# Optimization experiments

Measured on AMD Instinct MI355X. Metric: run time of the kernel, lower is better.

The kernel has to match this reference:

```python
import jax, jax.numpy as jnp
import numpy as np

N, E, D, R = 50000, 600000, 128, 8


def rgcn_conv(x, src, dst, etype, W, root, bias):
    """PyG-style RGCNConv with mean aggregation per relation.
    x: [N, Din]; W: [R, Din, Dout]; root: [Din, Dout]; bias: [Dout]."""
    n = x.shape[0]
    r = W.shape[0]
    # Transform once per relation at node level (cheaper than per-edge matmul).
    xw = jnp.einsum('nd,rdo->rno', x, W)  # [R, N, Dout]
    # Per-(relation, target) edge counts for mean normalization.
    seg = etype * n + dst                  # combined segment id in [0, R*N)
    counts = jax.ops.segment_sum(jnp.ones(src.shape, dtype=x.dtype), seg,
                                 num_segments=r * n)
    norm = 1.0 / jnp.maximum(counts[seg], 1.0)   # [E]
    msg = xw[etype, src] * norm[:, None]          # gather per edge, [E, Dout]
    agg = jax.ops.segment_sum(msg, dst, num_segments=n)  # scatter-add, [N, Dout]
    return agg + x @ root + bias


def setup_inputs() -> dict:
    key = jax.random.key(0)
    ks = jax.random.split(key, 16)
    s = 1.0 / np.sqrt(D)
    inp = {
        'x': jax.random.normal(ks[0], (N, D), dtype=jnp.float32),
        'edge_index': jax.random.randint(ks[1], (2, E), 0, N, dtype=jnp.int32),
        'edge_type': jax.random.randint(ks[2], (E,), 0, R, dtype=jnp.int32),
        'W1': jax.random.normal(ks[3], (R, D, D), dtype=jnp.float32) * s,
        'root1': jax.random.normal(ks[4], (D, D), dtype=jnp.float32) * s,
        'b1': jnp.zeros((D,), dtype=jnp.float32),
        'W2': jax.random.normal(ks[5], (R, D, D), dtype=jnp.float32) * s,
        'root2': jax.random.normal(ks[6], (D, D), dtype=jnp.float32) * s,
        'b2': jnp.zeros((D,), dtype=jnp.float32),
        'W3': jax.random.normal(ks[7], (R, D, D), dtype=jnp.float32) * s,
        'root3': jax.random.normal(ks[8], (D, D), dtype=jnp.float32) * s,
        'b3': jnp.zeros((D,), dtype=jnp.float32),
        'res_w': jax.random.normal(ks[9], (D, D), dtype=jnp.float32) * s,
        'res_b': jnp.zeros((D,), dtype=jnp.float32),
    }
    return inp


def reference(x, edge_index, edge_type, W1, root1, b1, W2, root2, b2,
              W3, root3, b3, res_w, res_b):
    src, dst = edge_index[0], edge_index[1]
    res = x @ res_w + res_b
    h = jax.nn.relu(rgcn_conv(x, src, dst, edge_type, W1, root1, b1))
    h = res + jax.nn.relu(h)
    h = jax.nn.relu(rgcn_conv(h, src, dst, edge_type, W2, root2, b2))
    h = res + jax.nn.relu(h)
    h = jax.nn.relu(rgcn_conv(h, src, dst, edge_type, W3, root3, b3))
    h = res + jax.nn.relu(h)
    # Dropout(0.05) is identity in eval mode.
    return h
```

## Files before the change

### kernel.cpp

```cpp
#include <hip/hip_runtime.h>
#include <hip/hip_bf16.h>

#define NN 50000
#define EE 600000
#define RR 8
#define NSEG (NN*RR)
#define NB_SCAN ((NSEG + 1023)/1024)

typedef unsigned int u32;
typedef __attribute__((ext_vector_type(8))) short bf16x8;
typedef __attribute__((ext_vector_type(4))) float f32x4;
typedef __attribute__((ext_vector_type(4))) u32 u32x4;

__device__ inline unsigned short f2bf(float f){
  u32 u = __float_as_uint(f);
  u32 r = (u + 0x7fffu + ((u >> 16) & 1u)) >> 16;
  return (unsigned short)r;
}
__device__ inline float bf2f(unsigned short b){ return __uint_as_float((u32)b << 16); }

#define GLD16(g, l)  __builtin_amdgcn_global_load_lds( \
    (const __attribute__((address_space(1))) void*)(g), \
    (__attribute__((address_space(3))) void*)(l), 16, 0, 0)

__global__ void cvt_k(const float* __restrict__ in, unsigned short* __restrict__ out, int n4){
  int i = blockIdx.x * 256 + threadIdx.x;
  if (i >= n4) return;
  float4 v = ((const float4*)in)[i];
  ushort4 o;
  o.x = f2bf(v.x); o.y = f2bf(v.y); o.z = f2bf(v.z); o.w = f2bf(v.w);
  ((ushort4*)out)[i] = o;
}

__global__ void pack_k(const float* __restrict__ Wrel, const float* __restrict__ root,
                       short* __restrict__ Bp, int nk32, int krel){
  int tid = blockIdx.x * 256 + threadIdx.x;
  if (tid >= nk32 * 512) return;
  int lane = tid & 63;
  int nf   = (tid >> 6) & 7;
  int k32  = tid >> 9;
  int col  = nf * 16 + (lane & 15);
  short vals[8];
#pragma unroll
  for (int i = 0; i < 8; ++i){
    int kk = k32 * 32 + ((lane >> 4) << 3) + i;
    float f = (kk < krel) ? Wrel[(size_t)kk * 128 + col]
                          : root[(size_t)(kk - krel) * 128 + col];
    vals[i] = (short)f2bf(f);
  }
  *(bf16x8*)(Bp + (size_t)tid * 8) = *(const bf16x8*)vals;
}

__global__ void count_k(const int* __restrict__ dst, const int* __restrict__ et,
                        u32* __restrict__ cnt){
  int e = blockIdx.x * 256 + threadIdx.x;
  if (e >= EE) return;
  atomicAdd(&cnt[(size_t)et[e] * NN + dst[e]], 1u);
}

__global__ void scan1_k(const u32* __restrict__ cnt, u32* __restrict__ offs, u32* __restrict__ bsum){
  __shared__ u32 s[512];
  int t = threadIdx.x;
  int base = blockIdx.x * 1024 + t * 4;
  u32 loc[4]; u32 sum = 0;
#pragma unroll
  for (int i = 0; i < 4; ++i){ loc[i] = (base + i < NSEG) ? cnt[base + i] : 0u; sum += loc[i]; }
  int pb = 0;
  s[t] = sum; __syncthreads();
  for (int off = 1; off < 256; off <<= 1){
    u32 v = s[pb * 256 + t];
    if (t >= off) v += s[pb * 256 + t - off];
    s[(pb ^ 1) * 256 + t] = v; pb ^= 1; __syncthreads();
  }
  u32 incl = s[pb * 256 + t];
  u32 excl = incl - sum;
  if (t == 255) bsum[blockIdx.x] = incl;
  u32 run = excl;
#pragma unroll
  for (int i = 0; i < 4; ++i){ if (base + i < NSEG) offs[base + i] = run; run += loc[i]; }
}

__global__ void scan2_k(u32* __restrict__ bsum){
  __shared__ u32 s[1024];
  int t = threadIdx.x;
  u32 v = (t < NB_SCAN) ? bsum[t] : 0u;
  int pb = 0;
  s[t] = v; __syncthreads();
  for (int off = 1; off < 512; off <<= 1){
    u32 x = s[pb * 512 + t];
    if (t >= off) x += s[pb * 512 + t - off];
    s[(pb ^ 1) * 512 + t] = x; pb ^= 1; __syncthreads();
  }
  u32 incl = s[pb * 512 + t];
  if (t < NB_SCAN) bsum[t] = incl - v;
}

__global__ void scan3_k(u32* __restrict__ offs, const u32* __restrict__ bsum){
  int t = threadIdx.x;
  int base = blockIdx.x * 1024 + t * 4;
  u32 add = bsum[blockIdx.x];
#pragma unroll
  for (int i = 0; i < 4; ++i){ if (base + i < NSEG) offs[base + i] += add; }
  if (blockIdx.x == 0 && t == 0) offs[NSEG] = EE;
}

__global__ void fill_k(const int* __restrict__ src, const int* __restrict__ dst,
                       const int* __restrict__ et, const u32* __restrict__ offs,
                       u32* __restrict__ cnt, int* __restrict__ elist){
  int e = blockIdx.x * 256 + threadIdx.x;
  if (e >= EE) return;
  int s = et[e] * NN + dst[e];
  u32 p = atomicSub(&cnt[s], 1u);
  elist[offs[s] + p - 1] = src[e];
}

__launch_bounds__(256, 4)
__global__ void resg_k(const unsigned short* __restrict__ xb, const short* __restrict__ Bp,
                       const float* __restrict__ rb, unsigned short* __restrict__ resb){
  const int tid = threadIdx.x;
  const int w = tid >> 6, l = tid & 63;
  const int sub = l >> 4, llr = l & 15;
  const int rowbase = blockIdx.x * 64 + w * 16;
  int vr = rowbase + llr; if (vr > NN - 1) vr = NN - 1;
  f32x4 acc[8] = {};
#pragma unroll
  for (int t = 0; t < 4; ++t){
    bf16x8 af = *(const bf16x8*)(xb + (size_t)vr * 128 + (t * 4 + sub) * 8);
    const short* bb = Bp + (size_t)(t * 8) * 512 + l * 8;
#pragma unroll
    for (int nf = 0; nf < 8; ++nf){
      bf16x8 bq = *(const bf16x8*)(bb + nf * 512);
      acc[nf] = __builtin_amdgcn_mfma_f32_16x16x32_bf16(af, bq, acc[nf], 0, 0, 0);
    }
  }
  const int lr = l >> 4, lc = l & 15;
#pragma unroll
  for (int nf = 0; nf < 8; ++nf){
    int col = nf * 16 + lc;
    float bv = rb[col];
#pragma unroll
    for (int r = 0; r < 4; ++r){
      int row = rowbase + lr * 4 + r;
      if (row < NN) resb[(size_t)row * 128 + col] = f2bf(acc[nf][r] + bv);
    }
  }
}

#define ACC1(P0, P1) do{ \
  _Pragma("unroll") \
  for (int i_ = 0; i_ < 4; ++i_){ \
    s[2*i_]     += __uint_as_float((P0)[i_] << 16); \
    s[2*i_+1]   += __uint_as_float((P0)[i_] & 0xffff0000u); \
    s[8+2*i_]   += __uint_as_float((P1)[i_] << 16); \
    s[8+2*i_+1] += __uint_as_float((P1)[i_] & 0xffff0000u); \
  } }while(0)

template<int OUTMODE>
__launch_bounds__(512, 4)
__global__ void fused_k(const u32* __restrict__ offs, const int* __restrict__ elist,
                        const unsigned short* __restrict__ h,
                        const short* __restrict__ Bp,
                        const float* __restrict__ bias,
                        const unsigned short* __restrict__ resb,
                        float* __restrict__ outf, unsigned short* __restrict__ outb){
  __shared__ short A[32 * 1152];
  char* Ab = (char*)A;
  const int tid = threadIdx.x;
  const int mbase = blockIdx.x * 32;

  {
    const int g = tid >> 3, ll8 = tid & 7;
    const unsigned short* hb = h + (size_t)ll8 * 16;
#pragma unroll 1
    for (int j = 0; j < 5; ++j){
      int task = j * 64 + g;
      if (task < 256){
        int r = task >> 5, row = task & 31;
        int v = mbase + row; if (v > NN - 1) v = NN - 1;
        size_t seg = (size_t)r * NN + v;
        u32 beg = offs[seg], end = offs[seg + 1];
        float s[16];
#pragma unroll
        for (int i = 0; i < 16; ++i) s[i] = 0.f;
        u32 e = beg;
        for (; e + 4 <= end; e += 4){
          int s0 = elist[e], s1 = elist[e+1], s2 = elist[e+2], s3 = elist[e+3];
          const unsigned short* r0 = hb + (size_t)s0 * 128;
          const unsigned short* r1 = hb + (size_t)s1 * 128;
          const unsigned short* r2 = hb + (size_t)s2 * 128;
          const unsigned short* r3 = hb + (size_t)s3 * 128;
          u32x4 p00 = *(const u32x4*)r0, p01 = *(const u32x4*)(r0 + 8);
          u32x4 p10 = *(const u32x4*)r1, p11 = *(const u32x4*)(r1 + 8);
          u32x4 p20 = *(const u32x4*)r2, p21 = *(const u32x4*)(r2 + 8);
          u32x4 p30 = *(const u32x4*)r3, p31 = *(const u32x4*)(r3 + 8);
          ACC1(p00, p01); ACC1(p10, p11); ACC1(p20, p21); ACC1(p30, p31);
        }
        if (e + 2 <= end){
          int s0 = elist[e], s1 = elist[e+1];
          const unsigned short* r0 = hb + (size_t)s0 * 128;
          const unsigned short* r1 = hb + (size_t)s1 * 128;
          u32x4 p00 = *(const u32x4*)r0, p01 = *(const u32x4*)(r0 + 8);
          u32x4 p10 = *(const u32x4*)r1, p11 = *(const u32x4*)(r1 + 8);
          ACC1(p00, p01); ACC1(p10, p11);
          e += 2;
        }
        if (e < end){
          int s0 = elist[e];
          const unsigned short* r0 = hb + (size_t)s0 * 128;
          u32x4 p00 = *(const u32x4*)r0, p01 = *(const u32x4*)(r0 + 8);
          ACC1(p00, p01);
        }
        u32 deg = end - beg;
        if (deg){
          float inv = 1.f / (float)deg;
#pragma unroll
          for (int i = 0; i < 16; ++i) s[i] *= inv;
        }
        u32x4 o0, o1;
#pragma unroll
        for (int i = 0; i < 4; ++i){
          o0[i] = (u32)f2bf(s[2*i])   | ((u32)f2bf(s[2*i+1])   << 16);
          o1[i] = (u32)f2bf(s[8+2*i]) | ((u32)f2bf(s[8+2*i+1]) << 16);
        }
        int k = row & 7;
        int sl = r * 16 + ll8 * 2;
        *(u32x4*)(Ab + row * 2304 + ((sl    ) ^ k) * 16) = o0;
        *(u32x4*)(Ab + row * 2304 + ((sl + 1) ^ k) * 16) = o1;
      } else if (task < 288){
        int row = task - 256;
        int v = mbase + row; if (v > NN - 1) v = NN - 1;
        const unsigned short* rp = h + (size_t)v * 128 + ll8 * 16;
        u32x4 o0 = *(const u32x4*)rp, o1 = *(const u32x4*)(rp + 8);
        int k = row & 7;
        int sl = 128 + ll8 * 2;
        *(u32x4*)(Ab + row * 2304 + ((sl    ) ^ k) * 16) = o0;
        *(u32x4*)(Ab + row * 2304 + ((sl + 1) ^ k) * 16) = o1;
      }
    }
  }
  __syncthreads();

  const int w = tid >> 6, l = tid & 63;
  const int sub = l >> 4, llr = l & 15;
  f32x4 acc[2] = {};
  const int k0 = llr & 7, k1 = (16 + llr) & 7;
#pragma unroll 6
  for (int kt = 0; kt < 18; ++kt){
#pragma unroll
    for (int t = 0; t < 2; ++t){
      int ks = kt * 8 + t * 4 + sub;
      bf16x8 af0 = *(const bf16x8*)(Ab + llr * 2304        + (ks ^ k0) * 16);
      bf16x8 af1 = *(const bf16x8*)(Ab + (16 + llr) * 2304 + (ks ^ k1) * 16);
      bf16x8 bq = *(const bf16x8*)(Bp + ((size_t)((kt * 2 + t) * 8 + w)) * 512 + l * 8);
      acc[0] = __builtin_amdgcn_mfma_f32_16x16x32_bf16(af0, bq, acc[0], 0, 0, 0);
      acc[1] = __builtin_amdgcn_mfma_f32_16x16x32_bf16(af1, bq, acc[1], 0, 0, 0);
    }
  }

  const int lr = l >> 4, lc = l & 15;
  int col = w * 16 + lc;
  float bv = bias[col];
#pragma unroll
  for (int mf = 0; mf < 2; ++mf){
#pragma unroll
    for (int r = 0; r < 4; ++r){
      int row = mbase + mf * 16 + lr * 4 + r;
      if (row < NN){
        float v = acc[mf][r] + bv;
        v = bf2f(resb[(size_t)row * 128 + col]) + fmaxf(v, 0.f);
        if (OUTMODE == 1) outb[(size_t)row * 128 + col] = f2bf(v);
        else              outf[(size_t)row * 128 + col] = v;
      }
    }
  }
}

extern "C" void kernel_launch(void* const* d_in, const int* in_sizes, int n_in,
                              void* d_out, int out_size, void* d_ws, size_t ws_size,
                              hipStream_t stream){
  const float* x  = (const float*)d_in[0];
  const int*   ei = (const int*)d_in[1];
  const int*   et = (const int*)d_in[2];
  const float* W1 = (const float*)d_in[3];
  const float* r1 = (const float*)d_in[4];
  const float* b1 = (const float*)d_in[5];
  const float* W2 = (const float*)d_in[6];
  const float* r2 = (const float*)d_in[7];
  const float* b2 = (const float*)d_in[8];
  const float* W3 = (const float*)d_in[9];
  const float* r3 = (const float*)d_in[10];
  const float* b3 = (const float*)d_in[11];
  const float* rw = (const float*)d_in[12];
  const float* rb = (const float*)d_in[13];
  const int* srcv = ei;
  const int* dstv = ei + EE;

  char* p = (char*)d_ws;
  auto take = [&](size_t b)->char*{ char* q = p; p += (b + 255) & ~(size_t)255; return q; };
  unsigned short* xb   = (unsigned short*)take((size_t)NN * 128 * 2);
  unsigned short* h1   = (unsigned short*)take((size_t)NN * 128 * 2);
  unsigned short* h2   = (unsigned short*)take((size_t)NN * 128 * 2);
  unsigned short* resb = (unsigned short*)take((size_t)NN * 128 * 2);
  short* Bp1 = (short*)take(36 * 4096 * 2);
  short* Bp2 = (short*)take(36 * 4096 * 2);
  short* Bp3 = (short*)take(36 * 4096 * 2);
  short* BpR = (short*)take(4 * 4096 * 2);
  u32* cnt   = (u32*)take((size_t)NSEG * 4);
  u32* offs  = (u32*)take((size_t)(NSEG + 1) * 4);
  int* elist = (int*)take((size_t)EE * 4);
  u32* bsum  = (u32*)take((size_t)NB_SCAN * 4);

  hipMemsetAsync(cnt, 0, (size_t)NSEG * 4, stream);

  cvt_k<<<(NN * 128 / 4 + 255) / 256, 256, 0, stream>>>(x, xb, NN * 128 / 4);
  pack_k<<<(36 * 512 + 255) / 256, 256, 0, stream>>>(W1, r1, Bp1, 36, 1024);
  pack_k<<<(36 * 512 + 255) / 256, 256, 0, stream>>>(W2, r2, Bp2, 36, 1024);
  pack_k<<<(36 * 512 + 255) / 256, 256, 0, stream>>>(W3, r3, Bp3, 36, 1024);
  pack_k<<<(4 * 512 + 255) / 256, 256, 0, stream>>>(nullptr, rw, BpR, 4, 0);

  count_k<<<(EE + 255) / 256, 256, 0, stream>>>(dstv, et, cnt);
  scan1_k<<<NB_SCAN, 256, 0, stream>>>(cnt, offs, bsum);
  scan2_k<<<1, 512, 0, stream>>>(bsum);
  scan3_k<<<NB_SCAN, 256, 0, stream>>>(offs, bsum);
  fill_k<<<(EE + 255) / 256, 256, 0, stream>>>(srcv, dstv, et, offs, cnt, elist);

  const int GB = (NN + 31) / 32;

  resg_k<<<(NN + 63) / 64, 256, 0, stream>>>(xb, BpR, rb, resb);

  fused_k<1><<<GB, 512, 0, stream>>>(offs, elist, xb, Bp1, b1, resb, nullptr, h1);
  fused_k<1><<<GB, 512, 0, stream>>>(offs, elist, h1, Bp2, b2, resb, nullptr, h2);
  fused_k<2><<<GB, 512, 0, stream>>>(offs, elist, h2, Bp3, b3, resb, (float*)d_out, nullptr);
}
```

Before: 316.6 us.

## Widen fused RGCN blocks to 1024 threads with one-shot gather and padded LDS

The fused gather+GEMM kernel now uses 1024 threads per block. Each 8-lane group handles exactly two (relation,row) segments with a software-prefetched gather loop, replacing the 5-iteration task loop. The LDS tile switches from an XOR swizzle to a padded row stride. Each wave now computes one 16x16 MFMA tile instead of two, and the four weight-packing launches are merged into one kernel. The aim is more parallelism and latency hiding in the gather and fewer launches, at the cost of a shallower per-segment unroll and lower per-wave MFMA reuse of the B fragments.

```diff
diff --git a/kernel.cpp b/kernel.cpp
--- a/kernel.cpp
+++ b/kernel.cpp
@@ -6,6 +6,7 @@
 #define RR 8
 #define NSEG (NN*RR)
 #define NB_SCAN ((NSEG + 1023)/1024)
+#define RSTRIDE 2320
 
 typedef unsigned int u32;
 typedef __attribute__((ext_vector_type(8))) short bf16x8;
@@ -18,10 +19,6 @@
   return (unsigned short)r;
 }
 __device__ inline float bf2f(unsigned short b){ return __uint_as_float((u32)b << 16); }
-
-#define GLD16(g, l)  __builtin_amdgcn_global_load_lds( \
-    (const __attribute__((address_space(1))) void*)(g), \
-    (__attribute__((address_space(3))) void*)(l), 16, 0, 0)
 
 __global__ void cvt_k(const float* __restrict__ in, unsigned short* __restrict__ out, int n4){
   int i = blockIdx.x * 256 + threadIdx.x;
@@ -32,13 +29,22 @@
   ((ushort4*)out)[i] = o;
 }
 
-__global__ void pack_k(const float* __restrict__ Wrel, const float* __restrict__ root,
-                       short* __restrict__ Bp, int nk32, int krel){
+__global__ void packall_k(const float* __restrict__ W1, const float* __restrict__ r1,
+                          const float* __restrict__ W2, const float* __restrict__ r2,
+                          const float* __restrict__ W3, const float* __restrict__ r3,
+                          const float* __restrict__ rw,
+                          short* __restrict__ Bp1, short* __restrict__ Bp2,
+                          short* __restrict__ Bp3, short* __restrict__ BpR){
   int tid = blockIdx.x * 256 + threadIdx.x;
-  if (tid >= nk32 * 512) return;
+  if (tid >= 112 * 512) return;
+  int unit = tid >> 9;
+  const float* Wrel; const float* root; short* Bp; int k32; int krel;
+  if      (unit < 36){ Wrel = W1; root = r1; Bp = Bp1; k32 = unit;       krel = 1024; }
+  else if (unit < 72){ Wrel = W2; root = r2; Bp = Bp2; k32 = unit - 36;  krel = 1024; }
+  else if (unit <108){ Wrel = W3; root = r3; Bp = Bp3; k32 = unit - 72;  krel = 1024; }
+  else               { Wrel = rw; root = rw; Bp = BpR; k32 = unit - 108; krel = 0;    }
   int lane = tid & 63;
   int nf   = (tid >> 6) & 7;
-  int k32  = tid >> 9;
   int col  = nf * 16 + (lane & 15);
   short vals[8];
 #pragma unroll
@@ -48,7 +54,7 @@
                           : root[(size_t)(kk - krel) * 128 + col];
     vals[i] = (short)f2bf(f);
   }
-  *(bf16x8*)(Bp + (size_t)tid * 8) = *(const bf16x8*)vals;
+  *(bf16x8*)(Bp + (size_t)(k32 * 512 + (tid & 511)) * 8) = *(const bf16x8*)vals;
 }
 
 __global__ void count_k(const int* __restrict__ dst, const int* __restrict__ et,
@@ -156,121 +162,102 @@
   } }while(0)
 
 template<int OUTMODE>
-__launch_bounds__(512, 4)
+__launch_bounds__(1024, 8)
 __global__ void fused_k(const u32* __restrict__ offs, const int* __restrict__ elist,
                         const unsigned short* __restrict__ h,
                         const short* __restrict__ Bp,
                         const float* __restrict__ bias,
                         const unsigned short* __restrict__ resb,
                         float* __restrict__ outf, unsigned short* __restrict__ outb){
-  __shared__ short A[32 * 1152];
-  char* Ab = (char*)A;
+  __shared__ char Ab[32 * RSTRIDE];
   const int tid = threadIdx.x;
   const int mbase = blockIdx.x * 32;
 
   {
     const int g = tid >> 3, ll8 = tid & 7;
     const unsigned short* hb = h + (size_t)ll8 * 16;
-#pragma unroll 1
-    for (int j = 0; j < 5; ++j){
-      int task = j * 64 + g;
-      if (task < 256){
-        int r = task >> 5, row = task & 31;
-        int v = mbase + row; if (v > NN - 1) v = NN - 1;
-        size_t seg = (size_t)r * NN + v;
-        u32 beg = offs[seg], end = offs[seg + 1];
-        float s[16];
-#pragma unroll
-        for (int i = 0; i < 16; ++i) s[i] = 0.f;
-        u32 e = beg;
-        for (; e + 4 <= end; e += 4){
-          int s0 = elist[e], s1 = elist[e+1], s2 = elist[e+2], s3 = elist[e+3];
-          const unsigned short* r0 = hb + (size_t)s0 * 128;
-          const unsigned short* r1 = hb + (size_t)s1 * 128;
-          const unsigned short* r2 = hb + (size_t)s2 * 128;
-          const unsigned short* r3 = hb + (size_t)s3 * 128;
-          u32x4 p00 = *(const u32x4*)r0, p01 = *(const u32x4*)(r0 + 8);
-          u32x4 p10 = *(const u32x4*)r1, p11 = *(const u32x4*)(r1 + 8);
-          u32x4 p20 = *(const u32x4*)r2, p21 = *(const u32x4*)(r2 + 8);
-          u32x4 p30 = *(const u32x4*)r3, p31 = *(const u32x4*)(r3 + 8);
-          ACC1(p00, p01); ACC1(p10, p11); ACC1(p20, p21); ACC1(p30, p31);
-        }
-        if (e + 2 <= end){
-          int s0 = elist[e], s1 = elist[e+1];
-          const unsigned short* r0 = hb + (size_t)s0 * 128;
-          const unsigned short* r1 = hb + (size_t)s1 * 128;
-          u32x4 p00 = *(const u32x4*)r0, p01 = *(const u32x4*)(r0 + 8);
-          u32x4 p10 = *(const u32x4*)r1, p11 = *(const u32x4*)(r1 + 8);
-          ACC1(p00, p01); ACC1(p10, p11);
-          e += 2;
-        }
-        if (e < end){
-          int s0 = elist[e];
-          const unsigned short* r0 = hb + (size_t)s0 * 128;
-          u32x4 p00 = *(const u32x4*)r0, p01 = *(const u32x4*)(r0 + 8);
-          ACC1(p00, p01);
-        }
-        u32 deg = end - beg;
-        if (deg){
-          float inv = 1.f / (float)deg;
-#pragma unroll
-          for (int i = 0; i < 16; ++i) s[i] *= inv;
-        }
-        u32x4 o0, o1;
-#pragma unroll
-        for (int i = 0; i < 4; ++i){
-          o0[i] = (u32)f2bf(s[2*i])   | ((u32)f2bf(s[2*i+1])   << 16);
-          o1[i] = (u32)f2bf(s[8+2*i]) | ((u32)f2bf(s[8+2*i+1]) << 16);
-        }
-        int k = row & 7;
-        int sl = r * 16 + ll8 * 2;
-        *(u32x4*)(Ab + row * 2304 + ((sl    ) ^ k) * 16) = o0;
-        *(u32x4*)(Ab + row * 2304 + ((sl + 1) ^ k) * 16) = o1;
-      } else if (task < 288){
-        int row = task - 256;
-        int v = mbase + row; if (v > NN - 1) v = NN - 1;
-        const unsigned short* rp = h + (size_t)v * 128 + ll8 * 16;
-        u32x4 o0 = *(const u32x4*)rp, o1 = *(const u32x4*)(rp + 8);
-        int k = row & 7;
-        int sl = 128 + ll8 * 2;
-        *(u32x4*)(Ab + row * 2304 + ((sl    ) ^ k) * 16) = o0;
-        *(u32x4*)(Ab + row * 2304 + ((sl + 1) ^ k) * 16) = o1;
-      }
+    int r0 = g >> 5, row0 = g & 31;
+    int t1 = g + 128;
+    int r1 = t1 >> 5, row1 = t1 & 31;
+    int v0 = mbase + row0; if (v0 > NN - 1) v0 = NN - 1;
+    int v1 = mbase + row1; if (v1 > NN - 1) v1 = NN - 1;
+    size_t sg0 = (size_t)r0 * NN + v0, sg1 = (size_t)r1 * NN + v1;
+    u32 b0 = offs[sg0], e0 = offs[sg0 + 1];
+    u32 b1 = offs[sg1], e1 = offs[sg1 + 1];
+    int fs0 = (b0 < e0) ? elist[b0] : 0;
+    int fs1 = (b1 < e1) ? elist[b1] : 0;
+
+#define GATHER(BEG, END, FS, ROW, RSEG) do{ \
+    float s[16]; \
+    _Pragma("unroll") for (int i_ = 0; i_ < 16; ++i_) s[i_] = 0.f; \
+    u32 deg_ = (END) - (BEG); \
+    if (deg_){ \
+      const unsigned short* rp_ = hb + (size_t)(FS) * 128; \
+      u32x4 c0_ = *(const u32x4*)rp_, c1_ = *(const u32x4*)(rp_ + 8); \
+      for (u32 e_ = (BEG) + 1; e_ < (END); ++e_){ \
+        int nv_ = elist[e_]; \
+        const unsigned short* np_ = hb + (size_t)nv_ * 128; \
+        u32x4 n0_ = *(const u32x4*)np_, n1_ = *(const u32x4*)(np_ + 8); \
+        ACC1(c0_, c1_); \
+        c0_ = n0_; c1_ = n1_; \
+      } \
+      ACC1(c0_, c1_); \
+      float inv_ = __builtin_amdgcn_rcpf((float)deg_); \
+      _Pragma("unroll") for (int i_ = 0; i_ < 16; ++i_) s[i_] *= inv_; \
+    } \
+    u32x4 o0_, o1_; \
+    _Pragma("unroll") \
+    for (int i_ = 0; i_ < 4; ++i_){ \
+      o0_[i_] = (u32)f2bf(s[2*i_])   | ((u32)f2bf(s[2*i_+1])   << 16); \
+      o1_[i_] = (u32)f2bf(s[8+2*i_]) | ((u32)f2bf(s[8+2*i_+1]) << 16); \
+    } \
+    char* wp_ = Ab + (ROW) * RSTRIDE + ((RSEG) * 16 + ll8 * 2) * 16; \
+    *(u32x4*)wp_ = o0_; \
+    *(u32x4*)(wp_ + 16) = o1_; \
+  }while(0)
+
+    GATHER(b0, e0, fs0, row0, r0);
+    GATHER(b1, e1, fs1, row1, r1);
+#undef GATHER
+    if (g < 32){
+      int row = g;
+      int v = mbase + row; if (v > NN - 1) v = NN - 1;
+      const unsigned short* rp = h + (size_t)v * 128 + ll8 * 16;
+      u32x4 o0 = *(const u32x4*)rp, o1 = *(const u32x4*)(rp + 8);
+      char* wp = Ab + row * RSTRIDE + (128 + ll8 * 2) * 16;
+      *(u32x4*)wp = o0;
+      *(u32x4*)(wp + 16) = o1;
     }
   }
   __syncthreads();
 
   const int w = tid >> 6, l = tid & 63;
+  const int mf = w >> 3, nf = w & 7;
   const int sub = l >> 4, llr = l & 15;
-  f32x4 acc[2] = {};
-  const int k0 = llr & 7, k1 = (16 + llr) & 7;
+  const int rowb = mf * 16 + llr;
+  f32x4 acc = {};
 #pragma unroll 6
   for (int kt = 0; kt < 18; ++kt){
 #pragma unroll
     for (int t = 0; t < 2; ++t){
       int ks = kt * 8 + t * 4 + sub;
-      bf16x8 af0 = *(const bf16x8*)(Ab + llr * 2304        + (ks ^ k0) * 16);
-      bf16x8 af1 = *(const bf16x8*)(Ab + (16 + llr) * 2304 + (ks ^ k1) * 16);
-      bf16x8 bq = *(const bf16x8*)(Bp + ((size_t)((kt * 2 + t) * 8 + w)) * 512 + l * 8);
-      acc[0] = __builtin_amdgcn_mfma_f32_16x16x32_bf16(af0, bq, acc[0], 0, 0, 0);
-      acc[1] = __builtin_amdgcn_mfma_f32_16x16x32_bf16(af1, bq, acc[1], 0, 0, 0);
+      bf16x8 af = *(const bf16x8*)(Ab + rowb * RSTRIDE + ks * 16);
+      bf16x8 bq = *(const bf16x8*)(Bp + ((size_t)((kt * 2 + t) * 8 + nf)) * 512 + l * 8);
+      acc = __builtin_amdgcn_mfma_f32_16x16x32_bf16(af, bq, acc, 0, 0, 0);
     }
   }
 
   const int lr = l >> 4, lc = l & 15;
-  int col = w * 16 + lc;
+  int col = nf * 16 + lc;
   float bv = bias[col];
 #pragma unroll
-  for (int mf = 0; mf < 2; ++mf){
-#pragma unroll
-    for (int r = 0; r < 4; ++r){
-      int row = mbase + mf * 16 + lr * 4 + r;
-      if (row < NN){
-        float v = acc[mf][r] + bv;
-        v = bf2f(resb[(size_t)row * 128 + col]) + fmaxf(v, 0.f);
-        if (OUTMODE == 1) outb[(size_t)row * 128 + col] = f2bf(v);
-        else              outf[(size_t)row * 128 + col] = v;
-      }
+  for (int r = 0; r < 4; ++r){
+    int row = mbase + mf * 16 + lr * 4 + r;
+    if (row < NN){
+      float v = acc[r] + bv;
+      v = bf2f(resb[(size_t)row * 128 + col]) + fmaxf(v, 0.f);
+      if (OUTMODE == 1) outb[(size_t)row * 128 + col] = f2bf(v);
+      else              outf[(size_t)row * 128 + col] = v;
     }
   }
 }
@@ -313,10 +300,8 @@
   hipMemsetAsync(cnt, 0, (size_t)NSEG * 4, stream);
 
   cvt_k<<<(NN * 128 / 4 + 255) / 256, 256, 0, stream>>>(x, xb, NN * 128 / 4);
-  pack_k<<<(36 * 512 + 255) / 256, 256, 0, stream>>>(W1, r1, Bp1, 36, 1024);
-  pack_k<<<(36 * 512 + 255) / 256, 256, 0, stream>>>(W2, r2, Bp2, 36, 1024);
-  pack_k<<<(36 * 512 + 255) / 256, 256, 0, stream>>>(W3, r3, Bp3, 36, 1024);
-  pack_k<<<(4 * 512 + 255) / 256, 256, 0, stream>>>(nullptr, rw, BpR, 4, 0);
+  packall_k<<<(112 * 512 + 255) / 256, 256, 0, stream>>>(W1, r1, W2, r2, W3, r3, rw,
+                                                         Bp1, Bp2, Bp3, BpR);
 
   count_k<<<(EE + 255) / 256, 256, 0, stream>>>(dstv, et, cnt);
   scan1_k<<<NB_SCAN, 256, 0, stream>>>(cnt, offs, bsum);
@@ -328,7 +313,7 @@
 
   resg_k<<<(NN + 63) / 64, 256, 0, stream>>>(xb, BpR, rb, resb);
 
-  fused_k<1><<<GB, 512, 0, stream>>>(offs, elist, xb, Bp1, b1, resb, nullptr, h1);
-  fused_k<1><<<GB, 512, 0, stream>>>(offs, elist, h1, Bp2, b2, resb, nullptr, h2);
-  fused_k<2><<<GB, 512, 0, stream>>>(offs, elist, h2, Bp3, b3, resb, (float*)d_out, nullptr);
-}
+  fused_k<1><<<GB, 1024, 0, stream>>>(offs, elist, xb, Bp1, b1, resb, nullptr, h1);
+  fused_k<1><<<GB, 1024, 0, stream>>>(offs, elist, h1, Bp2, b2, resb, nullptr, h2);
+  fused_k<2><<<GB, 1024, 0, stream>>>(offs, elist, h2, Bp3, b3, resb, (float*)d_out, nullptr);
+}
```

Result: faster. 309.8 us (-2.1%).
